# Kernel tuning notes

Hardware: AMD Instinct MI355X
Metric: run time of the kernel (lower is better)

The kernel has to match this reference:

```python
import jax, jax.numpy as jnp
import numpy as np

N = 50000
E = 800000
H = 128
K_CONVS = 3
K_HOPS = 3


def setup_inputs() -> dict:
    key = jax.random.key(0)
    ks = jax.random.split(key, 8)
    x = jax.random.normal(ks[0], (N, H), dtype=jnp.float32)
    edge_index = jax.random.randint(ks[1], (2, E), 0, N, dtype=jnp.int64)
    s = 1.0 / np.sqrt(H)
    # MPlayer edge MLP: Linear(2H->H), LeakyReLU(0.2), Linear(H->H)
    W1 = jax.random.normal(ks[2], (2 * H, H), dtype=jnp.float32) * (1.0 / np.sqrt(2 * H))
    b1 = jnp.zeros((H,), jnp.float32)
    W2 = jax.random.normal(ks[3], (H, H), dtype=jnp.float32) * s
    b2 = jnp.zeros((H,), jnp.float32)
    # TAGConv stack: K_CONVS layers, each with K_HOPS+1 weight mats [H,H] + bias
    tag_w = jax.random.normal(ks[4], (K_CONVS, K_HOPS + 1, H, H), dtype=jnp.float32) * s
    tag_b = jnp.zeros((K_CONVS, H), jnp.float32)
    return {"x": x, "edge_index": edge_index, "W1": W1, "b1": b1,
            "W2": W2, "b2": b2, "tag_w": tag_w, "tag_b": tag_b}


def _mp_layer(x, src, dst, W1, b1, W2, b2):
    # gather -> concat -> 2-layer MLP per edge -> scatter-add at dst
    h = jnp.concatenate([x[dst], x[src]], axis=-1)  # [E, 2H] (x_i=dst, x_j=src)
    h = jax.nn.leaky_relu(h @ W1 + b1, negative_slope=0.2)
    m = h @ W2 + b2
    return jax.ops.segment_sum(m, dst, num_segments=N)


def _tag_conv(x, src, dst, norm, Ws, b):
    # out = sum_k A_norm^k x @ W_k + b  (PyG TAGConv, add_self_loops=False)
    out = x @ Ws[0]
    for k in range(1, Ws.shape[0]):
        x = jax.ops.segment_sum(norm[:, None] * x[src], dst, num_segments=N)
        out = out + x @ Ws[k]
    return out + b


def reference(x, edge_index, W1, b1, W2, b2, tag_w, tag_b):
    src = edge_index[0]
    dst = edge_index[1]
    # symmetric gcn_norm without self-loops (degree counted at target=dst)
    deg = jax.ops.segment_sum(jnp.ones((E,), x.dtype), dst, num_segments=N)
    dinv = jnp.where(deg > 0, jax.lax.rsqrt(jnp.maximum(deg, 1e-12)), 0.0)
    norm = dinv[src] * dinv[dst]  # [E]

    x = _mp_layer(x, src, dst, W1, b1, W2, b2)
    for i in range(K_CONVS):
        x = _tag_conv(x, src, dst, norm, tag_w[i], tag_b[i])
        x = jax.nn.relu(x)
    return x
```

## Files before the change

kernel.cpp:

```cpp
#include <hip/hip_runtime.h>

#define NN 50000
#define NE 800000
#define HH 128
#define SCAN_BLK 256
#define NBLK ((NN + SCAN_BLK - 1) / SCAN_BLK)
#define NB8 ((NN + 7) / 8)

typedef _Float16 half8 __attribute__((ext_vector_type(8)));
typedef _Float16 half4 __attribute__((ext_vector_type(4)));
typedef float floatx16 __attribute__((ext_vector_type(16)));

static inline size_t align256(size_t x) { return (x + 255) & ~(size_t)255; }

__global__ void k_deg(const int* __restrict__ dst, int* __restrict__ deg) {
    int e = blockIdx.x * 256 + threadIdx.x;
    if (e < NE) atomicAdd(&deg[dst[e]], 1);
}

__global__ void k_bsum(const int* __restrict__ deg, int* __restrict__ part) {
    __shared__ int sd[SCAN_BLK];
    int t = threadIdx.x;
    int i = blockIdx.x * SCAN_BLK + t;
    sd[t] = (i < NN) ? deg[i] : 0;
    __syncthreads();
    for (int off = SCAN_BLK / 2; off > 0; off >>= 1) {
        if (t < off) sd[t] += sd[t + off];
        __syncthreads();
    }
    if (t == 0) part[blockIdx.x] = sd[0];
}

__global__ void k_scanpart(const int* __restrict__ part, int* __restrict__ partoff) {
    __shared__ int sd[SCAN_BLK];
    int t = threadIdx.x;
    int v = (t < NBLK) ? part[t] : 0;
    sd[t] = v;
    __syncthreads();
    for (int off = 1; off < SCAN_BLK; off <<= 1) {
        int add = (t >= off) ? sd[t - off] : 0;
        __syncthreads();
        sd[t] += add;
        __syncthreads();
    }
    if (t < NBLK) partoff[t] = sd[t] - v;
}

__global__ void k_apply(const int* __restrict__ deg, const int* __restrict__ partoff,
                        int* __restrict__ offsets, float* __restrict__ dinv) {
    __shared__ int sd[SCAN_BLK];
    int t = threadIdx.x;
    int i = blockIdx.x * SCAN_BLK + t;
    int v = (i < NN) ? deg[i] : 0;
    sd[t] = v;
    __syncthreads();
    for (int off = 1; off < SCAN_BLK; off <<= 1) {
        int add = (t >= off) ? sd[t - off] : 0;
        __syncthreads();
        sd[t] += add;
        __syncthreads();
    }
    if (i < NN) {
        offsets[i] = partoff[blockIdx.x] + sd[t] - v;
        dinv[i] = (v > 0) ? rsqrtf((float)v) : 0.0f;
    }
    if (i == 0) offsets[NN] = NE;
}

__global__ void k_fill(const int* __restrict__ src, const int* __restrict__ dst,
                       const int* __restrict__ offsets, int* __restrict__ cursor,
                       const float* __restrict__ dinv, uint2* __restrict__ epk) {
    int e = blockIdx.x * 256 + threadIdx.x;
    if (e >= NE) return;
    int s = src[e], d = dst[e];
    int pos = atomicAdd(&cursor[d], 1);
    int idx = offsets[d] + pos;
    float nv = dinv[s] * dinv[d];
    epk[idx] = make_uint2((unsigned)s, __float_as_uint(nv));
}

__global__ void k_cvt_x(const float* __restrict__ x, _Float16* __restrict__ xh) {
    int i = blockIdx.x * 256 + threadIdx.x;
    if (i * 4 < NN * HH) {
        float4 v = *(const float4*)(x + (size_t)i * 4);
        half4 h;
        h.x = (_Float16)v.x; h.y = (_Float16)v.y;
        h.z = (_Float16)v.z; h.w = (_Float16)v.w;
        *(half4*)(xh + (size_t)i * 4) = h;
    }
}

__global__ void k_cvt_w(const float* __restrict__ W1, const float* __restrict__ W2,
                        const float* __restrict__ tw,
                        _Float16* __restrict__ W1tP, _Float16* __restrict__ W1tQ,
                        _Float16* __restrict__ W2t, _Float16* __restrict__ TWt) {
    int i = blockIdx.x * 256 + threadIdx.x;
    if (i < 16384) {
        int c = i >> 7, k = i & 127;
        W1tP[c * 128 + k] = (_Float16)W1[k * 128 + c];
        W1tQ[c * 128 + k] = (_Float16)W1[(128 + k) * 128 + c];
    } else if (i < 32768) {
        int j = i - 16384;
        int c = j >> 7, k = j & 127;
        W2t[c * 128 + k] = (_Float16)W2[k * 128 + c];
    } else if (i < 32768 + 3 * 65536) {
        int j = i - 32768;
        int L = j >> 16;
        int c = (j >> 9) & 127;
        int k = j & 511;
        TWt[(size_t)L * 65536 + c * 512 + k] =
            (_Float16)tw[(size_t)L * 65536 + (size_t)(k >> 7) * 16384 + (size_t)(k & 127) * 128 + c];
    }
}

template <int KDIM, int HAS_BIAS, int HAS_DEG, int RELU, typename OutT>
__global__ __launch_bounds__(256) void k_mm(
    const _Float16* __restrict__ A, int lda,
    const _Float16* __restrict__ Bt,
    const float* __restrict__ bias, const int* __restrict__ deg,
    OutT* __restrict__ Out, int ldo, int nrows) {
    __shared__ _Float16 As[128 * 64];
    __shared__ _Float16 Bs[128 * 64];
    const int t = threadIdx.x;
    const int l = t & 63;
    const int w = t >> 6;
    const int wm = w >> 1, wn = w & 1;
    const int row0 = blockIdx.x * 128;

    floatx16 acc[2][2] = {};

    const int srow = t >> 3;
    const int sslot = t & 7;

    for (int c = 0; c < KDIM / 64; ++c) {
        __syncthreads();
#pragma unroll
        for (int p = 0; p < 4; ++p) {
            int r = srow + p * 32;
            int g = row0 + r;
            uint4 v = make_uint4(0, 0, 0, 0);
            if (g < nrows) v = *(const uint4*)(A + (size_t)g * lda + c * 64 + sslot * 8);
            *(uint4*)((char*)As + r * 128 + ((sslot * 16) ^ ((r & 7) << 4))) = v;
        }
#pragma unroll
        for (int p = 0; p < 4; ++p) {
            int r = srow + p * 32;
            uint4 v = *(const uint4*)(Bt + (size_t)r * KDIM + c * 64 + sslot * 8);
            *(uint4*)((char*)Bs + r * 128 + ((sslot * 16) ^ ((r & 7) << 4))) = v;
        }
        __syncthreads();
#pragma unroll
        for (int ks = 0; ks < 4; ++ks) {
            const int koff = ks * 32 + (l >> 5) * 16;
            half8 a0, a1, b0, b1;
            { int r = wm * 64 + (l & 31);      a0 = *(const half8*)((const char*)As + r * 128 + (koff ^ ((r & 7) << 4))); }
            { int r = wm * 64 + 32 + (l & 31); a1 = *(const half8*)((const char*)As + r * 128 + (koff ^ ((r & 7) << 4))); }
            { int r = wn * 64 + (l & 31);      b0 = *(const half8*)((const char*)Bs + r * 128 + (koff ^ ((r & 7) << 4))); }
            { int r = wn * 64 + 32 + (l & 31); b1 = *(const half8*)((const char*)Bs + r * 128 + (koff ^ ((r & 7) << 4))); }
            acc[0][0] = __builtin_amdgcn_mfma_f32_32x32x16_f16(a0, b0, acc[0][0], 0, 0, 0);
            acc[0][1] = __builtin_amdgcn_mfma_f32_32x32x16_f16(a0, b1, acc[0][1], 0, 0, 0);
            acc[1][0] = __builtin_amdgcn_mfma_f32_32x32x16_f16(a1, b0, acc[1][0], 0, 0, 0);
            acc[1][1] = __builtin_amdgcn_mfma_f32_32x32x16_f16(a1, b1, acc[1][1], 0, 0, 0);
        }
    }

#pragma unroll
    for (int mf = 0; mf < 2; ++mf) {
#pragma unroll
        for (int nf = 0; nf < 2; ++nf) {
            const int col = wn * 64 + nf * 32 + (l & 31);
            const float bc = HAS_BIAS ? bias[col] : 0.0f;
#pragma unroll
            for (int r = 0; r < 16; ++r) {
                int row = wm * 64 + mf * 32 + 4 * (l >> 5) + (r & 3) + 8 * (r >> 2);
                int g = row0 + row;
                if (g < nrows) {
                    float v = acc[mf][nf][r];
                    if (HAS_BIAS) v += (HAS_DEG ? (float)deg[g] : 1.0f) * bc;
                    if (RELU) v = fmaxf(v, 0.0f);
                    Out[(size_t)g * ldo + col] = (OutT)v;
                }
            }
        }
    }
}

__global__ __launch_bounds__(256) void k_edge_mp(_Float16* __restrict__ PQ,
                                                 const int* __restrict__ offsets,
                                                 const uint2* __restrict__ epk) {
    const int t = threadIdx.x;
    const int n = blockIdx.x * 8 + (t >> 5);
    if (n >= NN) return;
    const int lane = t & 31;
    const int beg = offsets[n], end = offsets[n + 1];
    half4 p4 = *(const half4*)(PQ + (size_t)n * 256 + lane * 4);
    const float p0 = (float)p4.x, p1 = (float)p4.y, p2 = (float)p4.z, p3 = (float)p4.w;
    float a0 = 0.f, a1 = 0.f, a2 = 0.f, a3 = 0.f;
    int i = beg;
#define LRELU4(vx, vy, vz, vw)                                        \
    a0 += ((vx) > 0.f) ? (vx) : 0.2f * (vx);                          \
    a1 += ((vy) > 0.f) ? (vy) : 0.2f * (vy);                          \
    a2 += ((vz) > 0.f) ? (vz) : 0.2f * (vz);                          \
    a3 += ((vw) > 0.f) ? (vw) : 0.2f * (vw);
    for (; i + 4 <= end; i += 4) {
        uint2 e0 = epk[i + 0], e1 = epk[i + 1], e2 = epk[i + 2], e3 = epk[i + 3];
        half4 q0 = *(const half4*)(PQ + (size_t)e0.x * 256 + 128 + lane * 4);
        half4 q1 = *(const half4*)(PQ + (size_t)e1.x * 256 + 128 + lane * 4);
        half4 q2 = *(const half4*)(PQ + (size_t)e2.x * 256 + 128 + lane * 4);
        half4 q3 = *(const half4*)(PQ + (size_t)e3.x * 256 + 128 + lane * 4);
        LRELU4(p0 + (float)q0.x, p1 + (float)q0.y, p2 + (float)q0.z, p3 + (float)q0.w)
        LRELU4(p0 + (float)q1.x, p1 + (float)q1.y, p2 + (float)q1.z, p3 + (float)q1.w)
        LRELU4(p0 + (float)q2.x, p1 + (float)q2.y, p2 + (float)q2.z, p3 + (float)q2.w)
        LRELU4(p0 + (float)q3.x, p1 + (float)q3.y, p2 + (float)q3.z, p3 + (float)q3.w)
    }
    for (; i < end; ++i) {
        uint2 e = epk[i];
        half4 q = *(const half4*)(PQ + (size_t)e.x * 256 + 128 + lane * 4);
        LRELU4(p0 + (float)q.x, p1 + (float)q.y, p2 + (float)q.z, p3 + (float)q.w)
    }
#undef LRELU4
    half4 o;
    o.x = (_Float16)a0; o.y = (_Float16)a1; o.z = (_Float16)a2; o.w = (_Float16)a3;
    *(half4*)(PQ + (size_t)n * 256 + lane * 4) = o;
}

__global__ __launch_bounds__(256) void k_spmm(const _Float16* __restrict__ Xin,
                                              _Float16* __restrict__ Yout,
                                              const int* __restrict__ offsets,
                                              const uint2* __restrict__ epk) {
    const int t = threadIdx.x;
    const int n = blockIdx.x * 8 + (t >> 5);
    if (n >= NN) return;
    const int lane = t & 31;
    const int beg = offsets[n], end = offsets[n + 1];
    float a0 = 0.f, a1 = 0.f, a2 = 0.f, a3 = 0.f;
    int i = beg;
    for (; i + 4 <= end; i += 4) {
        uint2 e0 = epk[i + 0], e1 = epk[i + 1], e2 = epk[i + 2], e3 = epk[i + 3];
        half4 v0 = *(const half4*)(Xin + (size_t)e0.x * 512 + lane * 4);
        half4 v1 = *(const half4*)(Xin + (size_t)e1.x * 512 + lane * 4);
        half4 v2 = *(const half4*)(Xin + (size_t)e2.x * 512 + lane * 4);
        half4 v3 = *(const half4*)(Xin + (size_t)e3.x * 512 + lane * 4);
        float n0 = __uint_as_float(e0.y), n1 = __uint_as_float(e1.y);
        float n2 = __uint_as_float(e2.y), n3 = __uint_as_float(e3.y);
        a0 += n0 * (float)v0.x + n1 * (float)v1.x + n2 * (float)v2.x + n3 * (float)v3.x;
        a1 += n0 * (float)v0.y + n1 * (float)v1.y + n2 * (float)v2.y + n3 * (float)v3.y;
        a2 += n0 * (float)v0.z + n1 * (float)v1.z + n2 * (float)v2.z + n3 * (float)v3.z;
        a3 += n0 * (float)v0.w + n1 * (float)v1.w + n2 * (float)v2.w + n3 * (float)v3.w;
    }
    for (; i < end; ++i) {
        uint2 e = epk[i];
        float nv = __uint_as_float(e.y);
        half4 v = *(const half4*)(Xin + (size_t)e.x * 512 + lane * 4);
        a0 += nv * (float)v.x; a1 += nv * (float)v.y;
        a2 += nv * (float)v.z; a3 += nv * (float)v.w;
    }
    half4 o;
    o.x = (_Float16)a0; o.y = (_Float16)a1; o.z = (_Float16)a2; o.w = (_Float16)a3;
    *(half4*)(Yout + (size_t)n * 512 + lane * 4) = o;
}

extern "C" void kernel_launch(void* const* d_in, const int* in_sizes, int n_in,
                              void* d_out, int out_size, void* d_ws, size_t ws_size,
                              hipStream_t stream) {
    const float* x  = (const float*)d_in[0];
    const int*   ei = (const int*)d_in[1];
    const float* W1 = (const float*)d_in[2];
    const float* b1 = (const float*)d_in[3];
    const float* W2 = (const float*)d_in[4];
    const float* b2 = (const float*)d_in[5];
    const float* tw = (const float*)d_in[6];
    const float* tb = (const float*)d_in[7];
    float* out = (float*)d_out;

    const int* srcp = ei;
    const int* dstp = ei + NE;

    char* p = (char*)d_ws;
    auto alloc = [&](size_t bytes) { char* r = p; p += align256(bytes); return r; };
    int*       deg     = (int*)alloc((size_t)NN * 4);
    int*       cursor  = (int*)alloc((size_t)NN * 4);
    int*       offsets = (int*)alloc((size_t)(NN + 1) * 4);
    float*     dinv    = (float*)alloc((size_t)NN * 4);
    int*       part    = (int*)alloc((size_t)NBLK * 4);
    int*       partoff = (int*)alloc((size_t)NBLK * 4);
    uint2*     epk     = (uint2*)alloc((size_t)NE * 8);
    _Float16*  xh      = (_Float16*)alloc((size_t)NN * HH * 2);
    _Float16*  PQ      = (_Float16*)alloc((size_t)NN * 256 * 2);
    _Float16*  X4      = (_Float16*)alloc((size_t)NN * 512 * 2);
    _Float16*  W1tP    = (_Float16*)alloc(16384 * 2);
    _Float16*  W1tQ    = (_Float16*)alloc(16384 * 2);
    _Float16*  W2t     = (_Float16*)alloc(16384 * 2);
    _Float16*  TWt     = (_Float16*)alloc((size_t)3 * 65536 * 2);

    hipMemsetAsync(deg, 0, (size_t)NN * 4, stream);
    hipMemsetAsync(cursor, 0, (size_t)NN * 4, stream);

    k_deg<<<(NE + 255) / 256, 256, 0, stream>>>(dstp, deg);
    k_bsum<<<NBLK, SCAN_BLK, 0, stream>>>(deg, part);
    k_scanpart<<<1, SCAN_BLK, 0, stream>>>(part, partoff);
    k_apply<<<NBLK, SCAN_BLK, 0, stream>>>(deg, partoff, offsets, dinv);
    k_fill<<<(NE + 255) / 256, 256, 0, stream>>>(srcp, dstp, offsets, cursor, dinv, epk);

    k_cvt_x<<<(NN * HH / 4 + 255) / 256, 256, 0, stream>>>(x, xh);
    k_cvt_w<<<(32768 + 3 * 65536 + 255) / 256, 256, 0, stream>>>(W1, W2, tw, W1tP, W1tQ, W2t, TWt);

    const int mmgrid = (NN + 127) / 128;

    k_mm<128, 1, 0, 0, _Float16><<<mmgrid, 256, 0, stream>>>(xh, HH, W1tP, b1, nullptr, PQ, 256, NN);
    k_mm<128, 0, 0, 0, _Float16><<<mmgrid, 256, 0, stream>>>(xh, HH, W1tQ, nullptr, nullptr, PQ + 128, 256, NN);
    k_edge_mp<<<NB8, 256, 0, stream>>>(PQ, offsets, epk);
    k_mm<128, 1, 1, 0, _Float16><<<mmgrid, 256, 0, stream>>>(PQ, 256, W2t, b2, deg, X4, 512, NN);

    for (int L = 0; L < 3; ++L) {
        const _Float16* Wt = TWt + (size_t)L * 65536;
        const float* bL = tb + (size_t)L * 128;
        k_spmm<<<NB8, 256, 0, stream>>>(X4 + 0,   X4 + 128, offsets, epk);
        k_spmm<<<NB8, 256, 0, stream>>>(X4 + 128, X4 + 256, offsets, epk);
        k_spmm<<<NB8, 256, 0, stream>>>(X4 + 256, X4 + 384, offsets, epk);
        if (L < 2) {
            k_mm<512, 1, 0, 1, _Float16><<<mmgrid, 256, 0, stream>>>(X4, 512, Wt, bL, nullptr, X4, 512, NN);
        } else {
            k_mm<512, 1, 0, 1, float><<<mmgrid, 256, 0, stream>>>(X4, 512, Wt, bL, nullptr, out, HH, NN);
        }
    }
}
```

Before: 529.4 us.

## Store node features in 32-column panels for cache-local sparse gathers

After: 741.4 us. 40.0% more time.

```diff
diff --git a/kernel.cpp b/kernel.cpp
--- a/kernel.cpp
+++ b/kernel.cpp
@@ -5,13 +5,20 @@
 #define HH 128
 #define SCAN_BLK 256
 #define NBLK ((NN + SCAN_BLK - 1) / SCAN_BLK)
-#define NB8 ((NN + 7) / 8)
+#define NODEBLKS ((NN + 31) / 32)
+#define PSZ ((size_t)NN * 32)
 
 typedef _Float16 half8 __attribute__((ext_vector_type(8)));
 typedef _Float16 half4 __attribute__((ext_vector_type(4)));
 typedef float floatx16 __attribute__((ext_vector_type(16)));
 
 static inline size_t align256(size_t x) { return (x + 255) & ~(size_t)255; }
+
+__device__ inline void ld_epk_nt(const uint2* p, unsigned& s, float& nv) {
+    unsigned long long u = __builtin_nontemporal_load((const unsigned long long*)p);
+    s = (unsigned)u;
+    nv = __uint_as_float((unsigned)(u >> 32));
+}
 
 __global__ void k_deg(const int* __restrict__ dst, int* __restrict__ deg) {
     int e = blockIdx.x * 256 + threadIdx.x;
@@ -113,7 +120,7 @@
     }
 }
 
-template <int KDIM, int HAS_BIAS, int HAS_DEG, int RELU, typename OutT>
+template <int KDIM, int A_MODE, int HAS_BIAS, int HAS_DEG, int RELU, int OUT_MODE, typename OutT>
 __global__ __launch_bounds__(256) void k_mm(
     const _Float16* __restrict__ A, int lda,
     const _Float16* __restrict__ Bt,
@@ -135,16 +142,24 @@
     for (int c = 0; c < KDIM / 64; ++c) {
         __syncthreads();
 #pragma unroll
-        for (int p = 0; p < 4; ++p) {
-            int r = srow + p * 32;
+        for (int p4 = 0; p4 < 4; ++p4) {
+            int r = srow + p4 * 32;
             int g = row0 + r;
             uint4 v = make_uint4(0, 0, 0, 0);
-            if (g < nrows) v = *(const uint4*)(A + (size_t)g * lda + c * 64 + sslot * 8);
+            if (g < nrows) {
+                if (A_MODE == 0) {
+                    v = *(const uint4*)(A + (size_t)g * lda + c * 64 + sslot * 8);
+                } else {
+                    int pan = c * 2 + (sslot >> 2);
+                    int jj8 = (sslot & 3) * 8;
+                    v = *(const uint4*)(A + ((size_t)pan * NN + g) * 32 + jj8);
+                }
+            }
             *(uint4*)((char*)As + r * 128 + ((sslot * 16) ^ ((r & 7) << 4))) = v;
         }
 #pragma unroll
-        for (int p = 0; p < 4; ++p) {
-            int r = srow + p * 32;
+        for (int p4 = 0; p4 < 4; ++p4) {
+            int r = srow + p4 * 32;
             uint4 v = *(const uint4*)(Bt + (size_t)r * KDIM + c * 64 + sslot * 8);
             *(uint4*)((char*)Bs + r * 128 + ((sslot * 16) ^ ((r & 7) << 4))) = v;
         }
@@ -178,23 +193,33 @@
                     float v = acc[mf][nf][r];
                     if (HAS_BIAS) v += (HAS_DEG ? (float)deg[g] : 1.0f) * bc;
                     if (RELU) v = fmaxf(v, 0.0f);
-                    Out[(size_t)g * ldo + col] = (OutT)v;
+                    if (OUT_MODE == 0) {
+                        Out[(size_t)g * ldo + col] = (OutT)v;
+                    } else {
+                        int pan = col >> 5, jj = col & 31;
+                        Out[((size_t)pan * NN + g) * 32 + jj] = (OutT)v;
+                    }
                 }
             }
         }
     }
 }
 
-__global__ __launch_bounds__(256) void k_edge_mp(_Float16* __restrict__ PQ,
+__global__ __launch_bounds__(256) void k_edge_mp(_Float16* __restrict__ Pp,
+                                                 const _Float16* __restrict__ Qp,
                                                  const int* __restrict__ offsets,
                                                  const uint2* __restrict__ epk) {
     const int t = threadIdx.x;
-    const int n = blockIdx.x * 8 + (t >> 5);
+    const int c = blockIdx.x / NODEBLKS;
+    const int n = (blockIdx.x % NODEBLKS) * 32 + (t >> 3);
     if (n >= NN) return;
-    const int lane = t & 31;
+    const int j4 = (t & 7) * 4;
+    _Float16* prow = Pp + ((size_t)c * NN + n) * 32 + j4;
+    const _Float16* Qb = Qp + (size_t)c * NN * 32;
+    half4 pv = __builtin_bit_cast(half4,
+        __builtin_nontemporal_load((const unsigned long long*)prow));
+    const float p0 = (float)pv.x, p1 = (float)pv.y, p2 = (float)pv.z, p3 = (float)pv.w;
     const int beg = offsets[n], end = offsets[n + 1];
-    half4 p4 = *(const half4*)(PQ + (size_t)n * 256 + lane * 4);
-    const float p0 = (float)p4.x, p1 = (float)p4.y, p2 = (float)p4.z, p3 = (float)p4.w;
     float a0 = 0.f, a1 = 0.f, a2 = 0.f, a3 = 0.f;
     int i = beg;
 #define LRELU4(vx, vy, vz, vw)                                        \
@@ -203,25 +228,30 @@
     a2 += ((vz) > 0.f) ? (vz) : 0.2f * (vz);                          \
     a3 += ((vw) > 0.f) ? (vw) : 0.2f * (vw);
     for (; i + 4 <= end; i += 4) {
-        uint2 e0 = epk[i + 0], e1 = epk[i + 1], e2 = epk[i + 2], e3 = epk[i + 3];
-        half4 q0 = *(const half4*)(PQ + (size_t)e0.x * 256 + 128 + lane * 4);
-        half4 q1 = *(const half4*)(PQ + (size_t)e1.x * 256 + 128 + lane * 4);
-        half4 q2 = *(const half4*)(PQ + (size_t)e2.x * 256 + 128 + lane * 4);
-        half4 q3 = *(const half4*)(PQ + (size_t)e3.x * 256 + 128 + lane * 4);
+        unsigned s0, s1, s2, s3; float d0, d1, d2, d3;
+        ld_epk_nt(&epk[i + 0], s0, d0);
+        ld_epk_nt(&epk[i + 1], s1, d1);
+        ld_epk_nt(&epk[i + 2], s2, d2);
+        ld_epk_nt(&epk[i + 3], s3, d3);
+        half4 q0 = *(const half4*)(Qb + (size_t)s0 * 32 + j4);
+        half4 q1 = *(const half4*)(Qb + (size_t)s1 * 32 + j4);
+        half4 q2 = *(const half4*)(Qb + (size_t)s2 * 32 + j4);
+        half4 q3 = *(const half4*)(Qb + (size_t)s3 * 32 + j4);
         LRELU4(p0 + (float)q0.x, p1 + (float)q0.y, p2 + (float)q0.z, p3 + (float)q0.w)
         LRELU4(p0 + (float)q1.x, p1 + (float)q1.y, p2 + (float)q1.z, p3 + (float)q1.w)
         LRELU4(p0 + (float)q2.x, p1 + (float)q2.y, p2 + (float)q2.z, p3 + (float)q2.w)
         LRELU4(p0 + (float)q3.x, p1 + (float)q3.y, p2 + (float)q3.z, p3 + (float)q3.w)
     }
     for (; i < end; ++i) {
-        uint2 e = epk[i];
-        half4 q = *(const half4*)(PQ + (size_t)e.x * 256 + 128 + lane * 4);
+        unsigned s; float d;
+        ld_epk_nt(&epk[i], s, d);
+        half4 q = *(const half4*)(Qb + (size_t)s * 32 + j4);
         LRELU4(p0 + (float)q.x, p1 + (float)q.y, p2 + (float)q.z, p3 + (float)q.w)
     }
 #undef LRELU4
     half4 o;
     o.x = (_Float16)a0; o.y = (_Float16)a1; o.z = (_Float16)a2; o.w = (_Float16)a3;
-    *(half4*)(PQ + (size_t)n * 256 + lane * 4) = o;
+    *(half4*)prow = o;
 }
 
 __global__ __launch_bounds__(256) void k_spmm(const _Float16* __restrict__ Xin,
@@ -229,35 +259,39 @@
                                               const int* __restrict__ offsets,
                                               const uint2* __restrict__ epk) {
     const int t = threadIdx.x;
-    const int n = blockIdx.x * 8 + (t >> 5);
+    const int c = blockIdx.x / NODEBLKS;
+    const int n = (blockIdx.x % NODEBLKS) * 32 + (t >> 3);
     if (n >= NN) return;
-    const int lane = t & 31;
+    const int j4 = (t & 7) * 4;
+    const _Float16* Xb = Xin + (size_t)c * NN * 32;
     const int beg = offsets[n], end = offsets[n + 1];
     float a0 = 0.f, a1 = 0.f, a2 = 0.f, a3 = 0.f;
     int i = beg;
     for (; i + 4 <= end; i += 4) {
-        uint2 e0 = epk[i + 0], e1 = epk[i + 1], e2 = epk[i + 2], e3 = epk[i + 3];
-        half4 v0 = *(const half4*)(Xin + (size_t)e0.x * 512 + lane * 4);
-        half4 v1 = *(const half4*)(Xin + (size_t)e1.x * 512 + lane * 4);
-        half4 v2 = *(const half4*)(Xin + (size_t)e2.x * 512 + lane * 4);
-        half4 v3 = *(const half4*)(Xin + (size_t)e3.x * 512 + lane * 4);
-        float n0 = __uint_as_float(e0.y), n1 = __uint_as_float(e1.y);
-        float n2 = __uint_as_float(e2.y), n3 = __uint_as_float(e3.y);
-        a0 += n0 * (float)v0.x + n1 * (float)v1.x + n2 * (float)v2.x + n3 * (float)v3.x;
-        a1 += n0 * (float)v0.y + n1 * (float)v1.y + n2 * (float)v2.y + n3 * (float)v3.y;
-        a2 += n0 * (float)v0.z + n1 * (float)v1.z + n2 * (float)v2.z + n3 * (float)v3.z;
-        a3 += n0 * (float)v0.w + n1 * (float)v1.w + n2 * (float)v2.w + n3 * (float)v3.w;
+        unsigned s0, s1, s2, s3; float d0, d1, d2, d3;
+        ld_epk_nt(&epk[i + 0], s0, d0);
+        ld_epk_nt(&epk[i + 1], s1, d1);
+        ld_epk_nt(&epk[i + 2], s2, d2);
+        ld_epk_nt(&epk[i + 3], s3, d3);
+        half4 v0 = *(const half4*)(Xb + (size_t)s0 * 32 + j4);
+        half4 v1 = *(const half4*)(Xb + (size_t)s1 * 32 + j4);
+        half4 v2 = *(const half4*)(Xb + (size_t)s2 * 32 + j4);
+        half4 v3 = *(const half4*)(Xb + (size_t)s3 * 32 + j4);
+        a0 += d0 * (float)v0.x + d1 * (float)v1.x + d2 * (float)v2.x + d3 * (float)v3.x;
+        a1 += d0 * (float)v0.y + d1 * (float)v1.y + d2 * (float)v2.y + d3 * (float)v3.y;
+        a2 += d0 * (float)v0.z + d1 * (float)v1.z + d2 * (float)v2.z + d3 * (float)v3.z;
+        a3 += d0 * (float)v0.w + d1 * (float)v1.w + d2 * (float)v2.w + d3 * (float)v3.w;
     }
     for (; i < end; ++i) {
-        uint2 e = epk[i];
-        float nv = __uint_as_float(e.y);
-        half4 v = *(const half4*)(Xin + (size_t)e.x * 512 + lane * 4);
-        a0 += nv * (float)v.x; a1 += nv * (float)v.y;
-        a2 += nv * (float)v.z; a3 += nv * (float)v.w;
+        unsigned s; float d;
+        ld_epk_nt(&epk[i], s, d);
+        half4 v = *(const half4*)(Xb + (size_t)s * 32 + j4);
+        a0 += d * (float)v.x; a1 += d * (float)v.y;
+        a2 += d * (float)v.z; a3 += d * (float)v.w;
     }
     half4 o;
     o.x = (_Float16)a0; o.y = (_Float16)a1; o.z = (_Float16)a2; o.w = (_Float16)a3;
-    *(half4*)(Yout + (size_t)n * 512 + lane * 4) = o;
+    *(half4*)(Yout + ((size_t)c * NN + n) * 32 + j4) = o;
 }
 
 extern "C" void kernel_launch(void* const* d_in, const int* in_sizes, int n_in,
@@ -286,8 +320,8 @@
     int*       partoff = (int*)alloc((size_t)NBLK * 4);
     uint2*     epk     = (uint2*)alloc((size_t)NE * 8);
     _Float16*  xh      = (_Float16*)alloc((size_t)NN * HH * 2);
-    _Float16*  PQ      = (_Float16*)alloc((size_t)NN * 256 * 2);
-    _Float16*  X4      = (_Float16*)alloc((size_t)NN * 512 * 2);
+    _Float16*  PQp     = (_Float16*)alloc((size_t)NN * 256 * 2);
+    _Float16*  X4p     = (_Float16*)alloc((size_t)NN * 512 * 2);
     _Float16*  W1tP    = (_Float16*)alloc(16384 * 2);
     _Float16*  W1tQ    = (_Float16*)alloc(16384 * 2);
     _Float16*  W2t     = (_Float16*)alloc(16384 * 2);
@@ -306,22 +340,23 @@
     k_cvt_w<<<(32768 + 3 * 65536 + 255) / 256, 256, 0, stream>>>(W1, W2, tw, W1tP, W1tQ, W2t, TWt);
 
     const int mmgrid = (NN + 127) / 128;
-
-    k_mm<128, 1, 0, 0, _Float16><<<mmgrid, 256, 0, stream>>>(xh, HH, W1tP, b1, nullptr, PQ, 256, NN);
-    k_mm<128, 0, 0, 0, _Float16><<<mmgrid, 256, 0, stream>>>(xh, HH, W1tQ, nullptr, nullptr, PQ + 128, 256, NN);
-    k_edge_mp<<<NB8, 256, 0, stream>>>(PQ, offsets, epk);
-    k_mm<128, 1, 1, 0, _Float16><<<mmgrid, 256, 0, stream>>>(PQ, 256, W2t, b2, deg, X4, 512, NN);
+    _Float16* Qp = PQp + 4 * PSZ;
+
+    k_mm<128, 0, 1, 0, 0, 1, _Float16><<<mmgrid, 256, 0, stream>>>(xh, HH, W1tP, b1, nullptr, PQp, 0, NN);
+    k_mm<128, 0, 0, 0, 0, 1, _Float16><<<mmgrid, 256, 0, stream>>>(xh, HH, W1tQ, nullptr, nullptr, Qp, 0, NN);
+    k_edge_mp<<<4 * NODEBLKS, 256, 0, stream>>>(PQp, Qp, offsets, epk);
+    k_mm<128, 1, 1, 1, 0, 1, _Float16><<<mmgrid, 256, 0, stream>>>(PQp, 0, W2t, b2, deg, X4p, 0, NN);
 
     for (int L = 0; L < 3; ++L) {
         const _Float16* Wt = TWt + (size_t)L * 65536;
         const float* bL = tb + (size_t)L * 128;
-        k_spmm<<<NB8, 256, 0, stream>>>(X4 + 0,   X4 + 128, offsets, epk);
-        k_spmm<<<NB8, 256, 0, stream>>>(X4 + 128, X4 + 256, offsets, epk);
-        k_spmm<<<NB8, 256, 0, stream>>>(X4 + 256, X4 + 384, offsets, epk);
+        k_spmm<<<4 * NODEBLKS, 256, 0, stream>>>(X4p + 0 * 4 * PSZ, X4p + 1 * 4 * PSZ, offsets, epk);
+        k_spmm<<<4 * NODEBLKS, 256, 0, stream>>>(X4p + 1 * 4 * PSZ, X4p + 2 * 4 * PSZ, offsets, epk);
+        k_spmm<<<4 * NODEBLKS, 256, 0, stream>>>(X4p + 2 * 4 * PSZ, X4p + 3 * 4 * PSZ, offsets, epk);
         if (L < 2) {
-            k_mm<512, 1, 0, 1, _Float16><<<mmgrid, 256, 0, stream>>>(X4, 512, Wt, bL, nullptr, X4, 512, NN);
+            k_mm<512, 1, 1, 0, 1, 1, _Float16><<<mmgrid, 256, 0, stream>>>(X4p, 0, Wt, bL, nullptr, X4p, 0, NN);
         } else {
-            k_mm<512, 1, 0, 1, float><<<mmgrid, 256, 0, stream>>>(X4, 512, Wt, bL, nullptr, out, HH, NN);
-        }
-    }
-}
+            k_mm<512, 1, 1, 0, 1, 0, float><<<mmgrid, 256, 0, stream>>>(X4p, 0, Wt, bL, nullptr, out, HH, NN);
+        }
+    }
+}
```
